# Kernel optimization log

Measured on AMD Instinct MI355X. Metric: run time of the kernel, lower is better.

Reference implementation:

```python
import jax, jax.numpy as jnp
import numpy as np

K = 3          # kernel_size (cubic)
S = 1          # stride
N_ITER = 3     # routing_iter
LAMBDA = 0.01  # inverse temperature used in M-step (CapsLayer default)
EPS = 1e-9


def _space_to_batch(x, k, s):
    # x: [B, D, H, W, C, ...] -> [B, oD, oH, oW, k^3 * C, ...]
    # patch ordering (kd, kh, kw, c) matches CapsLayer's gather+transpose+reshape.
    B, D, H, W, C = x.shape[:5]
    trail = x.shape[5:]
    oD = (D - k) // s + 1
    oH = (H - k) // s + 1
    oW = (W - k) // s + 1
    blocks = []
    for kd in range(k):
        for kh in range(k):
            for kw in range(k):
                blocks.append(x[:, kd:kd + oD * s:s, kh:kh + oH * s:s, kw:kw + oW * s:s])
    p = jnp.stack(blocks, axis=4)  # [B,oD,oH,oW,k^3,C,...]
    return p.reshape((B, oD, oH, oW, k ** 3 * C) + trail)


def _lse(x, axis):
    return jax.scipy.special.logsumexp(x, axis=axis, keepdims=True)


def _m_step(log_R, log_act, vote, bv, ba):
    # log_R: [...,I,O,1], log_act: [...,I,1,1], vote: [...,I,O,P]
    log_Ra = log_R + log_act
    R_sum = jnp.sum(jnp.exp(log_Ra), axis=-3, keepdims=True)        # [...,1,O,1]
    log_nR = log_Ra - _lse(log_Ra, axis=-3)                          # [...,I,O,1]
    pose = jnp.sum(vote * jnp.exp(log_nR), axis=-3, keepdims=True)   # [...,1,O,P]
    log_var = _lse(log_nR + jnp.log(jnp.square(vote - pose) + EPS), axis=-3)
    cost = R_sum * (bv + 0.5 * log_var)                              # [...,1,O,P]
    logit = LAMBDA * (ba - jnp.sum(cost, axis=-1, keepdims=True))    # [...,1,O,1]
    return pose, log_var, jax.nn.log_sigmoid(logit)


def _e_step(pose, log_var, log_act_out, vote):
    # per-dim Gaussian log-likelihood of votes under (pose, var)
    lp = -0.5 * (jnp.square(vote - pose) / jnp.exp(log_var) + log_var + jnp.log(2.0 * jnp.pi))
    lp = jnp.sum(lp, axis=-1, keepdims=True)                         # [...,I,O,1]
    logit = log_act_out + lp
    return logit - _lse(logit, axis=-2)                              # softmax over O


def _forward(pose, activation, W, beta_v, beta_a):
    pb = _space_to_batch(pose, K, S)            # [B,oD,oH,oW,I,4,4]
    ab = _space_to_batch(activation, K, S)      # [B,oD,oH,oW,I]
    # votes: W[i,o] @ pose_patch[...,i] -> [B,oD,oH,oW,I,O,4,4]
    vote = jnp.einsum('iork,bdhwikc->bdhwiorc', W, pb)
    vs = vote.shape
    vote = vote.reshape(vs[:-2] + (vs[-2] * vs[-1],))   # [...,I,O,16]
    nO = vote.shape[-2]
    log_act = jnp.log(ab + EPS)[..., None, None]        # [...,I,1,1]
    log_R = jnp.full(vote.shape[:-1] + (1,), -jnp.log(float(nO)), vote.dtype)
    bv = beta_v[None, None, None, None, None, :, :]     # [1,1,1,1,1,O,1]
    ba = beta_a[None, None, None, None, None, :, :]
    for t in range(N_ITER):
        v = vote if t == N_ITER - 1 else jax.lax.stop_gradient(vote)
        p, log_var, log_a = _m_step(log_R, log_act, v, bv, ba)
        if t < N_ITER - 1:
            log_R = _e_step(p, log_var, log_a, jax.lax.stop_gradient(vote))
    out_pose = jnp.squeeze(p, axis=-3).reshape(vs[:4] + (vs[-3], vs[-2], vs[-1]))  # [B,oD,oH,oW,O,4,4]
    out_act = jnp.exp(jnp.squeeze(log_a, axis=(-3, -1)))                            # [B,oD,oH,oW,O]
    return out_pose, out_act


def setup_inputs() -> dict:
    key = jax.random.key(0)
    k1, k2, k3, k4, k5 = jax.random.split(key, 5)
    pose = jax.random.normal(k1, (1, 12, 12, 12, 8, 4, 4), dtype=jnp.float32)
    activation = jax.random.uniform(k2, (1, 12, 12, 12, 8), dtype=jnp.float32)
    W = jax.random.normal(k3, (216, 16, 4, 4), dtype=jnp.float32)
    beta_v = jax.random.normal(k4, (16, 1), dtype=jnp.float32)
    beta_a = jax.random.normal(k5, (16, 1), dtype=jnp.float32)
    return {"pose": pose, "activation": activation, "W": W, "beta_v": beta_v, "beta_a": beta_a}


def reference(pose, activation, W, beta_v, beta_a):
    return _forward(pose, activation, W, beta_v, beta_a)
```

## Files before the change

### kernel.cpp

```cpp
#include <hip/hip_runtime.h>
#include <hip/hip_fp16.h>

#define NITER 3
#define LAMBDA 0.01f
#define EPS 1e-9f
#define LOG2PI 1.8378770664093453f

#define DIN 12
#define CIN 8
#define NI 216
#define NO 16
#define NK 14
#define PPAD 20
#define RSTR 216

__global__ __launch_bounds__(256)
void caps_em_kernel(const float* __restrict__ pose,
                    const float* __restrict__ act,
                    const float* __restrict__ W,
                    const float* __restrict__ beta_v,
                    const float* __restrict__ beta_a,
                    float* __restrict__ out)
{
    __shared__ __align__(16) char uBuf[17280];
    float (*sPT)[PPAD]  = (float (*)[PPAD])uBuf;
    float (*sRaT)[RSTR] = (float (*)[RSTR])uBuf;
    __shared__ float sAct[NI];
    __shared__ __align__(16) float sPoseM[NO][16];
    __shared__ __align__(16) float sIvM[NO][16];
    __shared__ float sCo[NO];

    const int t = threadIdx.x;
    const int b = blockIdx.x;
    const int od = b / 100;
    const int rem = b - od * 100;
    const int oh = rem / 10;
    const int ow = rem - oh * 10;

    const int o = t >> 4;
    const int j = t & 15;

    for (int u = t; u < NI * 4; u += 256) {
        int i = u >> 2, q = u & 3;
        int ci = i & 7, n = i >> 3;
        int kw = n % 3, n2 = n / 3;
        int kh = n2 % 3, kd = n2 / 3;
        const float4 v = *(const float4*)&pose[((((od + kd) * DIN + (oh + kh)) * DIN + (ow + kw)) * CIN + ci) * 16 + q * 4];
        sPT[i][0 + q]  = v.x;
        sPT[i][4 + q]  = v.y;
        sPT[i][8 + q]  = v.z;
        sPT[i][12 + q] = v.w;
    }
    if (t < NI) {
        int i = t;
        int ci = i & 7, n = i >> 3;
        int kw = n % 3, n2 = n / 3;
        int kh = n2 % 3, kd = n2 / 3;
        sAct[i] = act[(((od + kd) * DIN + (oh + kh)) * DIN + (ow + kw)) * CIN + ci] + EPS;
    }
    const float bv_o = beta_v[o];
    const float ba_o = beta_a[o];
    __syncthreads();

    const float4* W4 = (const float4*)W;
    __half2 vop[NK][8];
#pragma unroll
    for (int k = 0; k < NK; ++k) {
        const int ip = min(j + 16 * k, NI - 1);
        const float4* Wp = W4 + (ip * 16 + o) * 4;
        const float4 w0 = Wp[0], w1 = Wp[1], w2 = Wp[2], w3 = Wp[3];
        float v16[16];
#pragma unroll
        for (int cc = 0; cc < 4; ++cc) {
            const float4 pt = *(const float4*)&sPT[ip][cc * 4];
            v16[0 * 4 + cc]  = fmaf(w0.w, pt.w, fmaf(w0.z, pt.z, fmaf(w0.y, pt.y, w0.x * pt.x)));
            v16[1 * 4 + cc]  = fmaf(w1.w, pt.w, fmaf(w1.z, pt.z, fmaf(w1.y, pt.y, w1.x * pt.x)));
            v16[2 * 4 + cc]  = fmaf(w2.w, pt.w, fmaf(w2.z, pt.z, fmaf(w2.y, pt.y, w2.x * pt.x)));
            v16[3 * 4 + cc]  = fmaf(w3.w, pt.w, fmaf(w3.z, pt.z, fmaf(w3.y, pt.y, w3.x * pt.x)));
        }
#pragma unroll
        for (int p = 0; p < 8; ++p) {
            vop[k][p] = __floats2half2_rn(v16[2 * p], v16[2 * p + 1]);
        }
    }

    const int b3 = (j >> 3) & 1, b2 = (j >> 2) & 1, b1 = (j >> 1) & 1;
    const bool lastPartial = (j >= 8);
    const int eL = (j >> 1) & 7;

    for (int it = 0; it < NITER; ++it) {
        float rak[NK];
        float rs = 0.f;
#pragma unroll
        for (int k = 0; k < NK; ++k) {
            const int ip = min(j + 16 * k, NI - 1);
            float ra = (it == 0) ? sAct[ip] * 0.0625f : sRaT[o][ip];
            if (k == NK - 1 && lastPartial) ra = 0.f;
            rak[k] = ra;
            rs += ra;
        }
        rs += __shfl_xor(rs, 8);
        rs += __shfl_xor(rs, 4);
        rs += __shfl_xor(rs, 2);
        rs += __shfl_xor(rs, 1);
        const float inv_rs = 1.0f / rs;

        float peA, ivA, lvA, peB, ivB, lvB;
#pragma unroll
        for (int h = 0; h < 2; ++h) {
            float m1[8], m2[8];
#pragma unroll
            for (int q = 0; q < 8; ++q) { m1[q] = 0.f; m2[q] = 0.f; }
#pragma unroll
            for (int k = 0; k < NK; ++k) {
                const float ra = rak[k];
#pragma unroll
                for (int p = 0; p < 4; ++p) {
                    const float2 f = __half22float2(vop[k][h * 4 + p]);
                    const float rv0 = ra * f.x;
                    const float rv1 = ra * f.y;
                    m1[2 * p]     += rv0;
                    m1[2 * p + 1] += rv1;
                    m2[2 * p]     = fmaf(rv0, f.x, m2[2 * p]);
                    m2[2 * p + 1] = fmaf(rv1, f.y, m2[2 * p + 1]);
                }
            }
#pragma unroll
            for (int q = 0; q < 4; ++q) {
                float s1 = b3 ? m1[q] : m1[q + 4];
                float s2 = b3 ? m2[q] : m2[q + 4];
                m1[q] = (b3 ? m1[q + 4] : m1[q]) + __shfl_xor(s1, 8);
                m2[q] = (b3 ? m2[q + 4] : m2[q]) + __shfl_xor(s2, 8);
            }
#pragma unroll
            for (int q = 0; q < 2; ++q) {
                float s1 = b2 ? m1[q] : m1[q + 2];
                float s2 = b2 ? m2[q] : m2[q + 2];
                m1[q] = (b2 ? m1[q + 2] : m1[q]) + __shfl_xor(s1, 4);
                m2[q] = (b2 ? m2[q + 2] : m2[q]) + __shfl_xor(s2, 4);
            }
            {
                float s1 = b1 ? m1[0] : m1[1];
                float s2 = b1 ? m2[0] : m2[1];
                m1[0] = (b1 ? m1[1] : m1[0]) + __shfl_xor(s1, 2);
                m2[0] = (b1 ? m2[1] : m2[0]) + __shfl_xor(s2, 2);
            }
            m1[0] += __shfl_xor(m1[0], 1);
            m2[0] += __shfl_xor(m2[0], 1);

            const float pe = m1[0] * inv_rs;
            const float ve = fmaxf(m2[0] * inv_rs - pe * pe, 0.0f) + EPS;
            if (h == 0) { peA = pe; ivA = 1.0f / ve; lvA = __logf(ve); }
            else        { peB = pe; ivB = 1.0f / ve; lvB = __logf(ve); }
        }

        float SL = lvA + lvB;
        SL += __shfl_xor(SL, 1);
        SL += __shfl_xor(SL, 2);
        SL += __shfl_xor(SL, 4);
        SL += __shfl_xor(SL, 8);
        SL *= 0.5f;

        const float cost  = rs * (16.0f * bv_o + 0.5f * SL);
        const float logit = LAMBDA * (ba_o - cost);

        if (it == NITER - 1) {
            if ((j & 1) == 0) {
                out[(b * NO + o) * 16 + eL]     = peA;
                out[(b * NO + o) * 16 + 8 + eL] = peB;
            }
            if (j == 0) out[256000 + b * NO + o] = 1.0f / (1.0f + __expf(-logit));
            return;
        }

        const float log_a = (logit >= 0.0f) ? -log1pf(__expf(-logit))
                                            : logit - log1pf(__expf(logit));
        if ((j & 1) == 0) {
            sPoseM[o][eL]     = peA;
            sPoseM[o][8 + eL] = peB;
            sIvM[o][eL]       = ivA;
            sIvM[o][8 + eL]   = ivB;
        }
        if (j == 0) sCo[o] = log_a - 0.5f * SL - 8.0f * LOG2PI;
        __syncthreads();

        float qacc[NK];
#pragma unroll
        for (int k = 0; k < NK; ++k) qacc[k] = 0.f;
#pragma unroll
        for (int h = 0; h < 2; ++h) {
            float pv[8], iv8[8];
            *(float4*)&pv[0]  = *(const float4*)&sPoseM[o][h * 8];
            *(float4*)&pv[4]  = *(const float4*)&sPoseM[o][h * 8 + 4];
            *(float4*)&iv8[0] = *(const float4*)&sIvM[o][h * 8];
            *(float4*)&iv8[4] = *(const float4*)&sIvM[o][h * 8 + 4];
#pragma unroll
            for (int k = 0; k < NK; ++k) {
                float q = qacc[k];
#pragma unroll
                for (int p = 0; p < 4; ++p) {
                    const float2 f = __half22float2(vop[k][h * 4 + p]);
                    const float d0 = f.x - pv[2 * p];
                    const float d1 = f.y - pv[2 * p + 1];
                    q = fmaf(d0 * d0, iv8[2 * p], q);
                    q = fmaf(d1 * d1, iv8[2 * p + 1], q);
                }
                qacc[k] = q;
            }
        }
        {
            const float Co = sCo[o];
#pragma unroll
            for (int k = 0; k < NK; ++k) {
                if (!(k == NK - 1 && lastPartial)) {
                    sRaT[o][j + 16 * k] = Co - 0.5f * qacc[k];
                }
            }
        }
        __syncthreads();

        if (t < NI) {
            float l[16];
            float mx = -1e30f;
#pragma unroll
            for (int oo = 0; oo < 16; ++oo) { l[oo] = sRaT[oo][t]; mx = fmaxf(mx, l[oo]); }
            float s = 0.f;
#pragma unroll
            for (int oo = 0; oo < 16; ++oo) { l[oo] = __expf(l[oo] - mx); s += l[oo]; }
            const float sc = sAct[t] / s;
#pragma unroll
            for (int oo = 0; oo < 16; ++oo) sRaT[oo][t] = sc * l[oo];
        }
        __syncthreads();
    }
}

extern "C" void kernel_launch(void* const* d_in, const int* in_sizes, int n_in,
                              void* d_out, int out_size, void* d_ws, size_t ws_size,
                              hipStream_t stream) {
    const float* pose = (const float*)d_in[0];
    const float* actv = (const float*)d_in[1];
    const float* W    = (const float*)d_in[2];
    const float* bv   = (const float*)d_in[3];
    const float* ba   = (const float*)d_in[4];
    float* out = (float*)d_out;
    caps_em_kernel<<<dim3(1000), dim3(256), 0, stream>>>(pose, actv, W, bv, ba, out);
}
```

Before: 147.2 us.

## Double threads per block and do the E-step softmax over outputs in registers

The block grows to 512 threads, with the output capsule index as the fast lane index, so each thread holds votes for 7 input capsules instead of 14. The softmax over outputs now runs inside a wavefront using shuffles, which removes the shared-memory R transpose and its two barriers. M-step partial moments are reduced across wavefronts through new shared buffers, and a 256-thread finalize pass computes pose, variance and activation. The aim is to halve register pressure and serial work per thread and raise occupancy, at the cost of extra shared-memory traffic and one more barrier-guarded reduction stage.

```diff
diff --git a/kernel.cpp b/kernel.cpp
--- a/kernel.cpp
+++ b/kernel.cpp
@@ -10,11 +10,10 @@
 #define CIN 8
 #define NI 216
 #define NO 16
-#define NK 14
+#define NK 7
 #define PPAD 20
-#define RSTR 216
-
-__global__ __launch_bounds__(256)
+
+__global__ __launch_bounds__(512)
 void caps_em_kernel(const float* __restrict__ pose,
                     const float* __restrict__ act,
                     const float* __restrict__ W,
@@ -22,13 +21,16 @@
                     const float* __restrict__ beta_a,
                     float* __restrict__ out)
 {
-    __shared__ __align__(16) char uBuf[17280];
-    float (*sPT)[PPAD]  = (float (*)[PPAD])uBuf;
-    float (*sRaT)[RSTR] = (float (*)[RSTR])uBuf;
+    __shared__ __align__(16) float sPT[NI][PPAD];
+    __shared__ __align__(16) float sM1[16][17][8];
+    __shared__ __align__(16) float sM2[16][17][8];
+    __shared__ float sRs[16][8];
     __shared__ float sAct[NI];
     __shared__ __align__(16) float sPoseM[NO][16];
     __shared__ __align__(16) float sIvM[NO][16];
     __shared__ float sCo[NO];
+    __shared__ float sBv[NO];
+    __shared__ float sBa[NO];
 
     const int t = threadIdx.x;
     const int b = blockIdx.x;
@@ -37,10 +39,10 @@
     const int oh = rem / 10;
     const int ow = rem - oh * 10;
 
-    const int o = t >> 4;
-    const int j = t & 15;
-
-    for (int u = t; u < NI * 4; u += 256) {
+    const int o = t & 15;
+    const int j = t >> 4;
+
+    for (int u = t; u < NI * 4; u += 512) {
         int i = u >> 2, q = u & 3;
         int ci = i & 7, n = i >> 3;
         int kw = n % 3, n2 = n / 3;
@@ -58,15 +60,14 @@
         int kh = n2 % 3, kd = n2 / 3;
         sAct[i] = act[(((od + kd) * DIN + (oh + kh)) * DIN + (ow + kw)) * CIN + ci] + EPS;
     }
-    const float bv_o = beta_v[o];
-    const float ba_o = beta_a[o];
+    if (t < NO) { sBv[t] = beta_v[t]; sBa[t] = beta_a[t]; }
     __syncthreads();
 
     const float4* W4 = (const float4*)W;
     __half2 vop[NK][8];
 #pragma unroll
     for (int k = 0; k < NK; ++k) {
-        const int ip = min(j + 16 * k, NI - 1);
+        const int ip = min(j + 32 * k, NI - 1);
         const float4* Wp = W4 + (ip * 16 + o) * 4;
         const float4 w0 = Wp[0], w1 = Wp[1], w2 = Wp[2], w3 = Wp[3];
         float v16[16];
@@ -84,28 +85,26 @@
         }
     }
 
-    const int b3 = (j >> 3) & 1, b2 = (j >> 2) & 1, b1 = (j >> 1) & 1;
-    const bool lastPartial = (j >= 8);
-    const int eL = (j >> 1) & 7;
+    const int b0 = j & 1;
+    const int b1v = (j >> 1) & 1;
+    const int w = j >> 2;
+    const int eb = b0 * 4 + b1v * 2;
+    const bool lastPartial = (j >= 24);
+
+    float rak[NK];
+#pragma unroll
+    for (int k = 0; k < NK; ++k) {
+        const int ip = min(j + 32 * k, NI - 1);
+        rak[k] = sAct[ip] * 0.0625f;
+        if (k == NK - 1 && lastPartial) rak[k] = 0.f;
+    }
 
     for (int it = 0; it < NITER; ++it) {
-        float rak[NK];
-        float rs = 0.f;
-#pragma unroll
-        for (int k = 0; k < NK; ++k) {
-            const int ip = min(j + 16 * k, NI - 1);
-            float ra = (it == 0) ? sAct[ip] * 0.0625f : sRaT[o][ip];
-            if (k == NK - 1 && lastPartial) ra = 0.f;
-            rak[k] = ra;
-            rs += ra;
-        }
-        rs += __shfl_xor(rs, 8);
-        rs += __shfl_xor(rs, 4);
-        rs += __shfl_xor(rs, 2);
-        rs += __shfl_xor(rs, 1);
-        const float inv_rs = 1.0f / rs;
-
-        float peA, ivA, lvA, peB, ivB, lvB;
+        float rsp = ((rak[0] + rak[1]) + (rak[2] + rak[3])) + ((rak[4] + rak[5]) + rak[6]);
+        rsp += __shfl_xor(rsp, 16);
+        rsp += __shfl_xor(rsp, 32);
+
+        float p1[2][2], p2[2][2];
 #pragma unroll
         for (int h = 0; h < 2; ++h) {
             float m1[8], m2[8];
@@ -127,111 +126,127 @@
             }
 #pragma unroll
             for (int q = 0; q < 4; ++q) {
-                float s1 = b3 ? m1[q] : m1[q + 4];
-                float s2 = b3 ? m2[q] : m2[q + 4];
-                m1[q] = (b3 ? m1[q + 4] : m1[q]) + __shfl_xor(s1, 8);
-                m2[q] = (b3 ? m2[q + 4] : m2[q]) + __shfl_xor(s2, 8);
+                float s1 = b0 ? m1[q] : m1[q + 4];
+                float s2 = b0 ? m2[q] : m2[q + 4];
+                m1[q] = (b0 ? m1[q + 4] : m1[q]) + __shfl_xor(s1, 16);
+                m2[q] = (b0 ? m2[q + 4] : m2[q]) + __shfl_xor(s2, 16);
             }
 #pragma unroll
             for (int q = 0; q < 2; ++q) {
-                float s1 = b2 ? m1[q] : m1[q + 2];
-                float s2 = b2 ? m2[q] : m2[q + 2];
-                m1[q] = (b2 ? m1[q + 2] : m1[q]) + __shfl_xor(s1, 4);
-                m2[q] = (b2 ? m2[q + 2] : m2[q]) + __shfl_xor(s2, 4);
-            }
-            {
-                float s1 = b1 ? m1[0] : m1[1];
-                float s2 = b1 ? m2[0] : m2[1];
-                m1[0] = (b1 ? m1[1] : m1[0]) + __shfl_xor(s1, 2);
-                m2[0] = (b1 ? m2[1] : m2[0]) + __shfl_xor(s2, 2);
-            }
-            m1[0] += __shfl_xor(m1[0], 1);
-            m2[0] += __shfl_xor(m2[0], 1);
-
-            const float pe = m1[0] * inv_rs;
-            const float ve = fmaxf(m2[0] * inv_rs - pe * pe, 0.0f) + EPS;
-            if (h == 0) { peA = pe; ivA = 1.0f / ve; lvA = __logf(ve); }
-            else        { peB = pe; ivB = 1.0f / ve; lvB = __logf(ve); }
-        }
-
-        float SL = lvA + lvB;
-        SL += __shfl_xor(SL, 1);
-        SL += __shfl_xor(SL, 2);
-        SL += __shfl_xor(SL, 4);
-        SL += __shfl_xor(SL, 8);
-        SL *= 0.5f;
-
-        const float cost  = rs * (16.0f * bv_o + 0.5f * SL);
-        const float logit = LAMBDA * (ba_o - cost);
+                float s1 = b1v ? m1[q] : m1[q + 2];
+                float s2 = b1v ? m2[q] : m2[q + 2];
+                m1[q] = (b1v ? m1[q + 2] : m1[q]) + __shfl_xor(s1, 32);
+                m2[q] = (b1v ? m2[q + 2] : m2[q]) + __shfl_xor(s2, 32);
+            }
+            p1[h][0] = m1[0]; p1[h][1] = m1[1];
+            p2[h][0] = m2[0]; p2[h][1] = m2[1];
+        }
+#pragma unroll
+        for (int h = 0; h < 2; ++h) {
+#pragma unroll
+            for (int q = 0; q < 2; ++q) {
+                sM1[h * 8 + eb + q][o][w] = p1[h][q];
+                sM2[h * 8 + eb + q][o][w] = p2[h][q];
+            }
+        }
+        if ((j & 3) == 0) sRs[o][w] = rsp;
+        __syncthreads();
 
         if (it == NITER - 1) {
-            if ((j & 1) == 0) {
-                out[(b * NO + o) * 16 + eL]     = peA;
-                out[(b * NO + o) * 16 + 8 + eL] = peB;
-            }
-            if (j == 0) out[256000 + b * NO + o] = 1.0f / (1.0f + __expf(-logit));
+            if (t < 256) {
+                const int o2 = t >> 4, e2 = t & 15;
+                const float4 a0 = *(const float4*)&sM1[e2][o2][0];
+                const float4 a1 = *(const float4*)&sM1[e2][o2][4];
+                const float4 c0 = *(const float4*)&sM2[e2][o2][0];
+                const float4 c1 = *(const float4*)&sM2[e2][o2][4];
+                const float m1s = ((a0.x + a0.y) + (a0.z + a0.w)) + ((a1.x + a1.y) + (a1.z + a1.w));
+                const float m2s = ((c0.x + c0.y) + (c0.z + c0.w)) + ((c1.x + c1.y) + (c1.z + c1.w));
+                float rs = 0.f;
+#pragma unroll
+                for (int ww = 0; ww < 8; ++ww) rs += sRs[o2][ww];
+                const float inv_rs = 1.0f / rs;
+                const float pe = m1s * inv_rs;
+                const float ve = fmaxf(m2s * inv_rs - pe * pe, 0.0f) + EPS;
+                float SL = __logf(ve);
+                SL += __shfl_xor(SL, 1);
+                SL += __shfl_xor(SL, 2);
+                SL += __shfl_xor(SL, 4);
+                SL += __shfl_xor(SL, 8);
+                const float cost  = rs * (16.0f * sBv[o2] + 0.5f * SL);
+                const float logit = LAMBDA * (sBa[o2] - cost);
+                out[(b * NO + o2) * 16 + e2] = pe;
+                if (e2 == 0) out[256000 + b * NO + o2] = 1.0f / (1.0f + __expf(-logit));
+            }
             return;
         }
-
-        const float log_a = (logit >= 0.0f) ? -log1pf(__expf(-logit))
-                                            : logit - log1pf(__expf(logit));
-        if ((j & 1) == 0) {
-            sPoseM[o][eL]     = peA;
-            sPoseM[o][8 + eL] = peB;
-            sIvM[o][eL]       = ivA;
-            sIvM[o][8 + eL]   = ivB;
-        }
-        if (j == 0) sCo[o] = log_a - 0.5f * SL - 8.0f * LOG2PI;
+        if (t < 256) {
+            const int o2 = t >> 4, e2 = t & 15;
+            const float4 a0 = *(const float4*)&sM1[e2][o2][0];
+            const float4 a1 = *(const float4*)&sM1[e2][o2][4];
+            const float4 c0 = *(const float4*)&sM2[e2][o2][0];
+            const float4 c1 = *(const float4*)&sM2[e2][o2][4];
+            const float m1s = ((a0.x + a0.y) + (a0.z + a0.w)) + ((a1.x + a1.y) + (a1.z + a1.w));
+            const float m2s = ((c0.x + c0.y) + (c0.z + c0.w)) + ((c1.x + c1.y) + (c1.z + c1.w));
+            float rs = 0.f;
+#pragma unroll
+            for (int ww = 0; ww < 8; ++ww) rs += sRs[o2][ww];
+            const float inv_rs = 1.0f / rs;
+            const float pe = m1s * inv_rs;
+            const float ve = fmaxf(m2s * inv_rs - pe * pe, 0.0f) + EPS;
+            float SL = __logf(ve);
+            SL += __shfl_xor(SL, 1);
+            SL += __shfl_xor(SL, 2);
+            SL += __shfl_xor(SL, 4);
+            SL += __shfl_xor(SL, 8);
+            const float cost  = rs * (16.0f * sBv[o2] + 0.5f * SL);
+            const float logit = LAMBDA * (sBa[o2] - cost);
+            const float log_a = (logit >= 0.0f) ? -log1pf(__expf(-logit))
+                                                : logit - log1pf(__expf(logit));
+            sPoseM[o2][e2] = pe;
+            sIvM[o2][e2]   = 1.0f / ve;
+            if (e2 == 0) sCo[o2] = log_a - 0.5f * SL - 8.0f * LOG2PI;
+        }
         __syncthreads();
 
-        float qacc[NK];
-#pragma unroll
-        for (int k = 0; k < NK; ++k) qacc[k] = 0.f;
-#pragma unroll
-        for (int h = 0; h < 2; ++h) {
-            float pv[8], iv8[8];
-            *(float4*)&pv[0]  = *(const float4*)&sPoseM[o][h * 8];
-            *(float4*)&pv[4]  = *(const float4*)&sPoseM[o][h * 8 + 4];
-            *(float4*)&iv8[0] = *(const float4*)&sIvM[o][h * 8];
-            *(float4*)&iv8[4] = *(const float4*)&sIvM[o][h * 8 + 4];
+        {
+            float pv[16], iv16[16];
+            *(float4*)&pv[0]    = *(const float4*)&sPoseM[o][0];
+            *(float4*)&pv[4]    = *(const float4*)&sPoseM[o][4];
+            *(float4*)&pv[8]    = *(const float4*)&sPoseM[o][8];
+            *(float4*)&pv[12]   = *(const float4*)&sPoseM[o][12];
+            *(float4*)&iv16[0]  = *(const float4*)&sIvM[o][0];
+            *(float4*)&iv16[4]  = *(const float4*)&sIvM[o][4];
+            *(float4*)&iv16[8]  = *(const float4*)&sIvM[o][8];
+            *(float4*)&iv16[12] = *(const float4*)&sIvM[o][12];
+            const float Co = sCo[o];
 #pragma unroll
             for (int k = 0; k < NK; ++k) {
-                float q = qacc[k];
-#pragma unroll
-                for (int p = 0; p < 4; ++p) {
-                    const float2 f = __half22float2(vop[k][h * 4 + p]);
+                float qf = 0.f;
+#pragma unroll
+                for (int p = 0; p < 8; ++p) {
+                    const float2 f = __half22float2(vop[k][p]);
                     const float d0 = f.x - pv[2 * p];
                     const float d1 = f.y - pv[2 * p + 1];
-                    q = fmaf(d0 * d0, iv8[2 * p], q);
-                    q = fmaf(d1 * d1, iv8[2 * p + 1], q);
+                    qf = fmaf(d0 * d0, iv16[2 * p], qf);
+                    qf = fmaf(d1 * d1, iv16[2 * p + 1], qf);
                 }
-                qacc[k] = q;
-            }
-        }
-        {
-            const float Co = sCo[o];
-#pragma unroll
-            for (int k = 0; k < NK; ++k) {
-                if (!(k == NK - 1 && lastPartial)) {
-                    sRaT[o][j + 16 * k] = Co - 0.5f * qacc[k];
-                }
-            }
-        }
-        __syncthreads();
-
-        if (t < NI) {
-            float l[16];
-            float mx = -1e30f;
-#pragma unroll
-            for (int oo = 0; oo < 16; ++oo) { l[oo] = sRaT[oo][t]; mx = fmaxf(mx, l[oo]); }
-            float s = 0.f;
-#pragma unroll
-            for (int oo = 0; oo < 16; ++oo) { l[oo] = __expf(l[oo] - mx); s += l[oo]; }
-            const float sc = sAct[t] / s;
-#pragma unroll
-            for (int oo = 0; oo < 16; ++oo) sRaT[oo][t] = sc * l[oo];
-        }
-        __syncthreads();
+                const float l = Co - 0.5f * qf;
+                float mx = l;
+                mx = fmaxf(mx, __shfl_xor(mx, 1));
+                mx = fmaxf(mx, __shfl_xor(mx, 2));
+                mx = fmaxf(mx, __shfl_xor(mx, 4));
+                mx = fmaxf(mx, __shfl_xor(mx, 8));
+                const float ex = __expf(l - mx);
+                float s = ex;
+                s += __shfl_xor(s, 1);
+                s += __shfl_xor(s, 2);
+                s += __shfl_xor(s, 4);
+                s += __shfl_xor(s, 8);
+                const int ip = min(j + 32 * k, NI - 1);
+                rak[k] = sAct[ip] * ex / s;
+                if (k == NK - 1 && lastPartial) rak[k] = 0.f;
+            }
+        }
     }
 }
 
@@ -244,5 +259,5 @@
     const float* bv   = (const float*)d_in[3];
     const float* ba   = (const float*)d_in[4];
     float* out = (float*)d_out;
-    caps_em_kernel<<<dim3(1000), dim3(256), 0, stream>>>(pose, actv, W, bv, ba, out);
+    caps_em_kernel<<<dim3(1000), dim3(512), 0, stream>>>(pose, actv, W, bv, ba, out);
 }
```

Measured after the change: 132.1 us. 10.2% less time.
